# Optimization experiments

Measured on AMD Instinct MI355X. Metric: run time of the kernel, lower is better.

Reference implementation:

```python
import jax, jax.numpy as jnp
import numpy as np
from jax import lax

T = 8
TAU = 2.0
ALPHA = 4.0   # spikingjelly surrogate.Sigmoid default alpha
EPS = 1e-5


def _kaiming(key, shape, fan_in):
    return jax.random.normal(key, shape, jnp.float32) * np.sqrt(2.0 / fan_in)


def setup_inputs() -> dict:
    key = jax.random.key(0)
    ks = jax.random.split(key, 16)
    d = {}
    d['x'] = jax.random.normal(ks[0], (128, 3, 32, 32), jnp.float32)
    convs = [('1', 32, 3), ('2', 32, 32), ('3', 64, 32), ('4', 64, 64), ('5', 128, 64), ('6', 128, 128)]
    for i, (s, co, ci) in enumerate(convs):
        d['w' + s] = _kaiming(ks[1 + i], (co, ci, 3, 3), ci * 9)
        d['b' + s] = jnp.zeros((co,), jnp.float32)
        d['g' + s] = jnp.ones((co,), jnp.float32)
        d['be' + s] = jnp.zeros((co,), jnp.float32)
    d['fc1_w'] = _kaiming(ks[7], (128, 2048), 2048)
    d['fc1_b'] = jnp.zeros((128,), jnp.float32)
    d['fc2_w'] = _kaiming(ks[8], (10, 128), 128)
    d['fc2_b'] = jnp.zeros((10,), jnp.float32)
    return d


def _conv2d(x, w, b):  # x [M,C,H,W], w [O,I,3,3], pad=1 stride=1
    y = lax.conv_general_dilated(x, w, (1, 1), ((1, 1), (1, 1)),
                                 dimension_numbers=('NCHW', 'OIHW', 'NCHW'))
    return y + b[None, :, None, None]


def _bn(x, g, be):  # training-mode BN over merged (T*N,H,W) batch
    m = x.mean(axis=(0, 2, 3))
    v = x.var(axis=(0, 2, 3))
    inv = g / jnp.sqrt(v + EPS)
    return x * inv[None, :, None, None] + (be - m * inv)[None, :, None, None]


def _lif(x_seq, th):
    # spikingjelly LIFNode defaults: decay_input=True, v_reset=0 (hard reset),
    # surrogate sigmoid gradient. x_seq: [T, ...]
    def step(v, x):
        v = v + (x - v) / TAU
        sig = jax.nn.sigmoid(ALPHA * (v - th))
        hard = (v >= th).astype(x.dtype)
        spike = lax.stop_gradient(hard - sig) + sig  # fwd: heaviside, bwd: sigmoid'
        return v * (1.0 - spike), spike
    return lax.scan(step, jnp.zeros_like(x_seq[0]), x_seq)[1]


def _maxpool(x):  # [M,C,H,W] -> 2x2 stride 2
    return lax.reduce_window(x, -jnp.inf, lax.max, (1, 1, 2, 2), (1, 1, 2, 2), 'VALID')


def _cbl(xs, w, b, g, be, th):  # conv-bn over merged TN, LIF scan over T
    t, n = xs.shape[0], xs.shape[1]
    m = xs.reshape((t * n,) + xs.shape[2:])
    y = _bn(_conv2d(m, w, b), g, be)
    return _lif(y.reshape((t, n) + y.shape[1:]), th)


def _pool_seq(xs):
    t, n = xs.shape[0], xs.shape[1]
    y = _maxpool(xs.reshape((t * n,) + xs.shape[2:]))
    return y.reshape((t, n) + y.shape[1:])


def _forward(x, w1, b1, g1, be1, w2, b2, g2, be2, w3, b3, g3, be3,
             w4, b4, g4, be4, w5, b5, g5, be5, w6, b6, g6, be6,
             fc1_w, fc1_b, fc2_w, fc2_b):
    th = 1.0
    xs = jnp.broadcast_to(x[None], (T,) + x.shape)  # [T,N,3,32,32]
    xs = _cbl(xs, w1, b1, g1, be1, th)
    xs = _cbl(xs, w2, b2, g2, be2, th)
    xs = _pool_seq(xs)                                # [T,N,32,16,16]
    xs = _cbl(xs, w3, b3, g3, be3, th)
    xs = _cbl(xs, w4, b4, g4, be4, th)
    xs = _pool_seq(xs)                                # [T,N,64,8,8]
    xs = _cbl(xs, w5, b5, g5, be5, th)
    xs = _cbl(xs, w6, b6, g6, be6, th)
    xs = _pool_seq(xs)                                # [T,N,128,4,4]
    t, n = xs.shape[0], xs.shape[1]
    f = xs.reshape(t, n, -1)                          # [T,N,2048]
    h = jnp.einsum('tnf,of->tno', f, fc1_w) + fc1_b
    h = _lif(h, 1.0)
    o = jnp.einsum('tnf,of->tno', h, fc2_w) + fc2_b
    o = _lif(o, 1.0)
    return o.mean(axis=0)                             # [N,10]


def reference(x, w1, b1, g1, be1, w2, b2, g2, be2, w3, b3, g3, be3,
              w4, b4, g4, be4, w5, b5, g5, be5, w6, b6, g6, be6,
              fc1_w, fc1_b, fc2_w, fc2_b):
    return _forward(x, w1, b1, g1, be1, w2, b2, g2, be2, w3, b3, g3, be3,
                    w4, b4, g4, be4, w5, b5, g5, be5, w6, b6, g6, be6,
                    fc1_w, fc1_b, fc2_w, fc2_b)
```

## Files before the change

### kernel.cpp

```cpp
#include <hip/hip_runtime.h>
#include <stdint.h>


#define T_STEPS 8
#define NBATCH 128

typedef __attribute__((ext_vector_type(8))) short short8;
typedef __attribute__((ext_vector_type(4))) float f32x4;

__device__ __forceinline__ uint16_t f2bf(float f) {
    uint32_t x = __float_as_uint(f);
    uint32_t r = x + 0x7FFFu + ((x >> 16) & 1u);
    return (uint16_t)(r >> 16);
}
__device__ __forceinline__ float bf2f(uint16_t h) {
    return __uint_as_float(((uint32_t)h) << 16);
}

__device__ __forceinline__ void tsplit(float v, uint16_t& h1, uint16_t& h2, uint16_t& h3) {
    h1 = f2bf(v);
    const float r1 = v - bf2f(h1);
    h2 = f2bf(r1);
    const float r2 = r1 - bf2f(h2);
    h3 = f2bf(r2);
}

__device__ __forceinline__ void prep_conv_one(const float* __restrict__ w,
                                              uint16_t* __restrict__ wp, int i, int CIN) {
    const int KC = CIN >> 5;
    const int sh = i % 9;
    const int ci = (i / 9) % CIN;
    const int co = i / (9 * CIN);
    uint16_t h1, h2, h3;
    tsplit(w[i], h1, h2, h3);
    uint16_t* base = wp + (size_t)((co >> 4) * KC + (ci >> 5)) * 14976
                        + sh * 1664 + (co & 15) * 104 + (ci & 31);
    base[0] = h1;
    base[32] = h2;
    base[64] = h3;
}

__device__ __forceinline__ void prep_fc1_one(const float* __restrict__ w,
                                             uint16_t* __restrict__ wp, int i) {
    const int kp = i & 2047;
    const int o = i >> 11;
    const int px = kp >> 7, c = kp & 127;
    uint16_t h1, h2, h3;
    tsplit(w[o * 2048 + c * 16 + px], h1, h2, h3);
    uint16_t* base = wp + (size_t)((o >> 4) * 64 + (kp >> 5)) * 1664
                        + (o & 15) * 104 + (kp & 31);
    base[0] = h1;
    base[32] = h2;
    base[64] = h3;
}

__global__ void prep_all_kernel(const float* __restrict__ W2, const float* __restrict__ W3,
                                const float* __restrict__ W4, const float* __restrict__ W5,
                                const float* __restrict__ W6, const float* __restrict__ F1,
                                uint16_t* __restrict__ P2, uint16_t* __restrict__ P3,
                                uint16_t* __restrict__ P4, uint16_t* __restrict__ P5,
                                uint16_t* __restrict__ P6, uint16_t* __restrict__ PF,
                                float* __restrict__ stats) {
    int i = blockIdx.x * blockDim.x + threadIdx.x;
    if (i < 1536) { stats[i] = 0.0f; return; }
    i -= 1536;
    if (i < 9216) { prep_conv_one(W2, P2, i, 32); return; }
    i -= 9216;
    if (i < 18432) { prep_conv_one(W3, P3, i, 32); return; }
    i -= 18432;
    if (i < 36864) { prep_conv_one(W4, P4, i, 64); return; }
    i -= 36864;
    if (i < 73728) { prep_conv_one(W5, P5, i, 64); return; }
    i -= 73728;
    if (i < 147456) { prep_conv_one(W6, P6, i, 128); return; }
    i -= 147456;
    if (i < 262144) prep_fc1_one(F1, PF, i);
}

__global__ void border_all_kernel(uint8_t* S1, uint8_t* S2, uint8_t* S3,
                                  uint8_t* S4, uint8_t* S5, uint8_t* S6) {
    int i = blockIdx.x * blockDim.x + threadIdx.x;
    uint8_t* s;
    int C, HP, WPP;
    if (i < 1081344) { s = S1; C = 32; HP = 34; WPP = 34; }
    else if ((i -= 1081344) < 557056) { s = S2; C = 32; HP = 18; WPP = 18; }
    else if ((i -= 557056) < 1114112) { s = S3; C = 64; HP = 18; WPP = 18; }
    else if ((i -= 1114112) < 589824) { s = S4; C = 64; HP = 10; WPP = 10; }
    else if ((i -= 589824) < 1179648) { s = S5; C = 128; HP = 10; WPP = 10; }
    else if ((i -= 1179648) < 655360) { s = S6; C = 128; HP = 6; WPP = 6; }
    else return;
    const int C4 = C >> 2;
    const int NB = 2 * WPP + 2 * (HP - 2);
    const int c4 = i % C4;
    const int b = (i / C4) % NB;
    const int img = i / (C4 * NB);
    int py, px;
    if (b < WPP) { py = 0; px = b; }
    else if (b < 2 * WPP) { py = HP - 1; px = b - WPP; }
    else { const int r = b - 2 * WPP; py = 1 + (r >> 1); px = (r & 1) ? (WPP - 1) : 0; }
    *(uint32_t*)&s[(size_t)img * (HP * WPP * C) + (py * WPP + px) * C + 4 * c4] = 0u;
}

__global__ __launch_bounds__(256) void conv1_kernel(
    const float* __restrict__ x, const float* __restrict__ w,
    const float* __restrict__ bias, float* __restrict__ y,
    float* __restrict__ ssum, float* __restrict__ ssq)
{
    __shared__ float tile[3][10][34];
    __shared__ float bnl[64];
    const int tid = threadIdx.x;
    const int m = blockIdx.x;
    const int y0 = blockIdx.y * 8;
    const int co = tid & 31;
    const int strip = tid >> 5;

    if (tid < 64) bnl[tid] = 0.0f;
    for (int i = tid; i < 3 * 10 * 34; i += 256) ((float*)tile)[i] = 0.0f;
    __syncthreads();

    {
        const int gy0 = (y0 == 0) ? 0 : y0 - 1;
        const int gy1 = (y0 + 8 > 31) ? 31 : y0 + 8;
        const int nrows = gy1 - gy0 + 1;
        for (int i = tid; i < 3 * nrows * 32; i += 256) {
            const int gx = i & 31;
            const int r = (i >> 5) % nrows;
            const int ci = i / (32 * nrows);
            const int gy = gy0 + r;
            tile[ci][gy - y0 + 1][gx + 1] =
                x[((size_t)m * 3 + ci) * 1024 + gy * 32 + gx];
        }
    }
    __syncthreads();

    float wr[27];
#pragma unroll
    for (int j = 0; j < 27; ++j) wr[j] = w[co * 27 + j];
    const float bv = bias[co];

    float lsum = 0.0f, lsq = 0.0f;
#pragma unroll
    for (int g = 0; g < 8; ++g) {
        float s[3][3][6];
#pragma unroll
        for (int ci = 0; ci < 3; ++ci)
#pragma unroll
            for (int ky = 0; ky < 3; ++ky)
#pragma unroll
                for (int c = 0; c < 6; ++c)
                    s[ci][ky][c] = tile[ci][g + ky][strip * 4 + c];
#pragma unroll
        for (int r = 0; r < 4; ++r) {
            float acc = bv;
#pragma unroll
            for (int ci = 0; ci < 3; ++ci)
#pragma unroll
                for (int ky = 0; ky < 3; ++ky)
#pragma unroll
                    for (int kx = 0; kx < 3; ++kx)
                        acc += s[ci][ky][r + kx] * wr[ci * 9 + ky * 3 + kx];
            const int lx = strip * 4 + r;
            y[(((size_t)m * 1024) + (y0 + g) * 32 + lx) * 32 + co] = acc;
            lsum += acc;
            lsq += acc * acc;
        }
    }
    atomicAdd(&bnl[co], lsum);
    atomicAdd(&bnl[32 + co], lsq);
    __syncthreads();
    if (tid < 32) atomicAdd(&ssum[tid], bnl[tid]);
    else if (tid < 64) atomicAdd(&ssq[tid - 32], bnl[tid]);
}

template <int CIN, int COUT, int H, int W, int ROWS, int IMPB, int NCO, int KSPLIT>
__global__ __launch_bounds__(256) void conv_mfma_kernel(
    const uint8_t* __restrict__ in, const uint16_t* __restrict__ wp,
    const float* __restrict__ bias, float* __restrict__ y,
    float* __restrict__ ssum, float* __restrict__ ssq)
{
    constexpr int KC = CIN / 32;
    constexpr int WPP = W + 2;
    constexpr int HW = H * W;
    constexpr int PXU16 = CIN + 8;
    constexpr int ISTR_B = (H + 2) * WPP * CIN;
    constexpr int RB = H / ROWS;
    constexpr int NSTRIP = IMPB * ROWS * W / 16;
    constexpr int MSPLIT = 4 / KSPLIT;
    constexpr int SPW = NSTRIP / MSPLIT;
    constexpr int TILE_U16 = IMPB * (ROWS + 2) * WPP * PXU16;
    constexpr int TILE_B = IMPB * (ROWS + 2) * WPP * CIN;
    constexpr int NIT = KC * 9;
    constexpr int ITW = NIT / KSPLIT;
    constexpr int CS = NCO * 16 + 1;
    static_assert(IMPB == 1 || ROWS == H, "impb needs full-image tiles");
    static_assert(NSTRIP % MSPLIT == 0 && NSTRIP % 4 == 0, "strips");
    static_assert(NIT % KSPLIT == 0, "ksplit");
    static_assert(TILE_B % 16 == 0, "tile u8 16B");
    static_assert(KSPLIT == 1 || TILE_U16 * 2 >= NSTRIP * 16 * CS * 4, "C fits");

    __shared__ __align__(16) uint16_t sp[TILE_U16];
    __shared__ float bn[NCO * 32];

    const int tid = threadIdx.x;
    const int lane = tid & 63;
    const int wav = tid >> 6;
    const int kg = wav / MSPLIT;
    const int mg = wav - kg * MSPLIT;
    const int col = lane & 15;
    const int quad = lane >> 4;

    const int m0 = (blockIdx.x / RB) * IMPB;
    const int ybase = (blockIdx.x % RB) * ROWS;

    if (tid < NCO * 32) bn[tid] = 0.0f;

    {
        const uint8_t* src = in + (size_t)m0 * ISTR_B + (size_t)ybase * WPP * CIN;
        for (int i = tid; i < TILE_B / 16; i += 256) {
            const uint4 v = ((const uint4*)src)[i];
            const int b = i * 16;
            const int px = b / CIN;
            const int ci = b - px * CIN;
            uint32_t* d = (uint32_t*)&sp[px * PXU16 + ci];
            d[0] = ((v.x & 1u) | (((v.x >> 8) & 1u) << 16)) * 0x3F80u;
            d[1] = (((v.x >> 16) & 1u) | (((v.x >> 24) & 1u) << 16)) * 0x3F80u;
            d[2] = ((v.y & 1u) | (((v.y >> 8) & 1u) << 16)) * 0x3F80u;
            d[3] = (((v.y >> 16) & 1u) | (((v.y >> 24) & 1u) << 16)) * 0x3F80u;
            d[4] = ((v.z & 1u) | (((v.z >> 8) & 1u) << 16)) * 0x3F80u;
            d[5] = (((v.z >> 16) & 1u) | (((v.z >> 24) & 1u) << 16)) * 0x3F80u;
            d[6] = ((v.w & 1u) | (((v.w >> 8) & 1u) << 16)) * 0x3F80u;
            d[7] = (((v.w >> 16) & 1u) | (((v.w >> 24) & 1u) << 16)) * 0x3F80u;
        }
    }
    __syncthreads();

    int abase[SPW];
#pragma unroll
    for (int s = 0; s < SPW; ++s) {
        const int p = (mg * SPW + s) * 16 + col;
        const int img = p / (ROWS * W);
        const int rem = p % (ROWS * W);
        abase[s] = ((img * (ROWS + 2) + rem / W) * WPP + rem % W) * PXU16 + quad * 8;
    }

    f32x4 acc[SPW][NCO];
#pragma unroll
    for (int s = 0; s < SPW; ++s)
#pragma unroll
        for (int j = 0; j < NCO; ++j) acc[s][j] = (f32x4)0.0f;

    const uint16_t* wbase = wp + ((size_t)blockIdx.y * NCO * KC) * 14976
                               + col * 104 + quad * 8;

    auto loadB = [&](short8 (&buf)[NCO][3], int it) {
        const int kc = it / 9, sh = it - kc * 9;
#pragma unroll
        for (int j = 0; j < NCO; ++j) {
            const uint16_t* p = wbase + (size_t)(j * KC + kc) * 14976 + sh * 1664;
            buf[j][0] = *(const short8*)p;
            buf[j][1] = *(const short8*)(p + 32);
            buf[j][2] = *(const short8*)(p + 64);
        }
    };
    auto mfmaStep = [&](short8 (&buf)[NCO][3], int it) {
        const int kc = it / 9, sh = it - kc * 9;
        const int dy = sh / 3, dx = sh - dy * 3;
        const int shoff = (dy * WPP + dx) * PXU16 + kc * 32;
#pragma unroll
        for (int s = 0; s < SPW; ++s) {
            const short8 a = *(const short8*)&sp[abase[s] + shoff];
#pragma unroll
            for (int j = 0; j < NCO; ++j) {
                f32x4 t = acc[s][j];
                t = __builtin_amdgcn_mfma_f32_16x16x32_bf16(a, buf[j][0], t, 0, 0, 0);
                t = __builtin_amdgcn_mfma_f32_16x16x32_bf16(a, buf[j][1], t, 0, 0, 0);
                t = __builtin_amdgcn_mfma_f32_16x16x32_bf16(a, buf[j][2], t, 0, 0, 0);
                acc[s][j] = t;
            }
        }
    };

    short8 bufA[NCO][3], bufB[NCO][3];
    const int it0 = kg * ITW, it1 = it0 + ITW;
    loadB(bufA, it0);
    int it = it0;
#pragma unroll 1
    for (; it + 2 <= it1; it += 2) {
        loadB(bufB, it + 1);
        mfmaStep(bufA, it);
        if (it + 2 < it1) loadB(bufA, it + 2);
        mfmaStep(bufB, it + 1);
    }
    if (it < it1) mfmaStep(bufA, it);

    float bv[NCO];
#pragma unroll
    for (int j = 0; j < NCO; ++j) bv[j] = bias[(blockIdx.y * NCO + j) * 16 + col];

    if constexpr (KSPLIT == 1) {
#pragma unroll
        for (int s = 0; s < SPW; ++s) {
            const int pb_ = (mg * SPW + s) * 16 + quad * 4;
            float sum[NCO], sq[NCO];
#pragma unroll
            for (int j = 0; j < NCO; ++j) { sum[j] = 0.0f; sq[j] = 0.0f; }
#pragma unroll
            for (int r = 0; r < 4; ++r) {
                const int p = pb_ + r;
                const int img = p / (ROWS * W);
                const int pxim = p % (ROWS * W) + ybase * W;
                float* yp = &y[((size_t)(m0 + img) * HW + pxim) * COUT
                               + blockIdx.y * NCO * 16 + col];
#pragma unroll
                for (int j = 0; j < NCO; ++j) {
                    const float v = acc[s][j][r] + bv[j];
                    yp[j * 16] = v;
                    sum[j] += v;
                    sq[j] += v * v;
                }
            }
#pragma unroll
            for (int j = 0; j < NCO; ++j) {
                float su = sum[j], s2 = sq[j];
                su += __shfl_xor(su, 16, 64);
                su += __shfl_xor(su, 32, 64);
                s2 += __shfl_xor(s2, 16, 64);
                s2 += __shfl_xor(s2, 32, 64);
                if (quad == 0) {
                    atomicAdd(&bn[j * 32 + col], su);
                    atomicAdd(&bn[j * 32 + 16 + col], s2);
                }
            }
        }
    } else {
        float* Csh = (float*)sp;
        __syncthreads();
        if (kg == 0) {
#pragma unroll
            for (int s = 0; s < SPW; ++s)
#pragma unroll
                for (int j = 0; j < NCO; ++j)
#pragma unroll
                    for (int r = 0; r < 4; ++r)
                        Csh[((mg * SPW + s) * 16 + quad * 4 + r) * CS + j * 16 + col]
                            = acc[s][j][r];
        }
        __syncthreads();
#pragma unroll
        for (int k = 1; k < KSPLIT; ++k) {
            if (kg == k) {
#pragma unroll
                for (int s = 0; s < SPW; ++s)
#pragma unroll
                    for (int j = 0; j < NCO; ++j)
#pragma unroll
                        for (int r = 0; r < 4; ++r)
                            Csh[((mg * SPW + s) * 16 + quad * 4 + r) * CS + j * 16 + col]
                                += acc[s][j][r];
            }
            __syncthreads();
        }
        constexpr int ES = NSTRIP / 4;
#pragma unroll
        for (int s2i = 0; s2i < ES; ++s2i) {
            const int gs = wav * ES + s2i;
            float sum[NCO], sq[NCO];
#pragma unroll
            for (int j = 0; j < NCO; ++j) { sum[j] = 0.0f; sq[j] = 0.0f; }
#pragma unroll
            for (int r = 0; r < 4; ++r) {
                const int p = gs * 16 + quad * 4 + r;
                const int img = p / (ROWS * W);
                const int pxim = p % (ROWS * W) + ybase * W;
                float* yp = &y[((size_t)(m0 + img) * HW + pxim) * COUT
                               + blockIdx.y * NCO * 16 + col];
#pragma unroll
                for (int j = 0; j < NCO; ++j) {
                    const float v = Csh[p * CS + j * 16 + col] + bv[j];
                    yp[j * 16] = v;
                    sum[j] += v;
                    sq[j] += v * v;
                }
            }
#pragma unroll
            for (int j = 0; j < NCO; ++j) {
                float su = sum[j], s2 = sq[j];
                su += __shfl_xor(su, 16, 64);
                su += __shfl_xor(su, 32, 64);
                s2 += __shfl_xor(s2, 16, 64);
                s2 += __shfl_xor(s2, 32, 64);
                if (quad == 0) {
                    atomicAdd(&bn[j * 32 + col], su);
                    atomicAdd(&bn[j * 32 + 16 + col], s2);
                }
            }
        }
    }
    __syncthreads();
    if (tid < NCO * 32) {
        const int j = tid >> 5, r = tid & 31;
        const int co0 = (blockIdx.y * NCO + j) * 16;
        if (r < 16) atomicAdd(&ssum[co0 + r], bn[j * 32 + r]);
        else atomicAdd(&ssq[co0 + r - 16], bn[j * 32 + r]);
    }
}

__global__ void bnlif1_pad_kernel(const float* __restrict__ y,
                                  const float* __restrict__ ssum,
                                  const float* __restrict__ ssq,
                                  const float* __restrict__ g,
                                  const float* __restrict__ be,
                                  uint8_t* __restrict__ s, float invM) {
    constexpr int OSTR = 34 * 34 * 32;
    const int i = blockIdx.x * blockDim.x + threadIdx.x;
    if (i >= NBATCH * 1024 * 8) return;
    const int c4 = i & 7;
    const int px = (i >> 3) & 1023;
    const int n = i >> 13;
    const int c0 = 4 * c4;
    float z[4], v[4];
    const float4 q = *(const float4*)&y[((size_t)n * 1024 + px) * 32 + c0];
    const float* qf = (const float*)&q;
#pragma unroll
    for (int c = 0; c < 4; ++c) {
        const float m = ssum[c0 + c] * invM;
        const float inv = g[c0 + c] / sqrtf(ssq[c0 + c] * invM - m * m + 1e-5f);
        z[c] = qf[c] * inv + (be[c0 + c] - m * inv);
        v[c] = 0.0f;
    }
    const int pyy = px >> 5, pxx = px & 31;
    const size_t obase = (size_t)n * OSTR + ((pyy + 1) * 34 + pxx + 1) * 32 + c0;
    const size_t ot = (size_t)NBATCH * OSTR;
#pragma unroll
    for (int t = 0; t < T_STEPS; ++t) {
        uint32_t pk = 0;
#pragma unroll
        for (int c = 0; c < 4; ++c) {
            v[c] += (z[c] - v[c]) * 0.5f;
            if (v[c] >= 1.0f) { v[c] = 0.0f; pk |= 1u << (8 * c); }
        }
        *(uint32_t*)&s[t * ot + obase] = pk;
    }
}

template <int C, int H, int W>
__global__ void bnlif_pad_kernel(const float* __restrict__ y,
                                 const float* __restrict__ ssum,
                                 const float* __restrict__ ssq,
                                 const float* __restrict__ g,
                                 const float* __restrict__ be,
                                 uint8_t* __restrict__ s, float invM) {
    constexpr int C4 = C / 4;
    constexpr int HW = H * W;
    constexpr int OSTR = (H + 2) * (W + 2) * C;
    const int i = blockIdx.x * blockDim.x + threadIdx.x;
    if (i >= NBATCH * HW * C4) return;
    const int c4 = i % C4;
    const int px = (i / C4) % HW;
    const int n = i / (C4 * HW);
    const int c0 = 4 * c4;
    float inv[4], sh[4], v[4];
#pragma unroll
    for (int c = 0; c < 4; ++c) {
        const float m = ssum[c0 + c] * invM;
        inv[c] = g[c0 + c] / sqrtf(ssq[c0 + c] * invM - m * m + 1e-5f);
        sh[c] = be[c0 + c] - m * inv[c];
        v[c] = 0.0f;
    }
    const size_t ybase = ((size_t)n * HW + px) * C + c0;
    const size_t tstride = (size_t)NBATCH * HW * C;
    const int pyy = px / W, pxx = px % W;
    const size_t obase = (size_t)n * OSTR + ((pyy + 1) * (W + 2) + pxx + 1) * C + c0;
    const size_t ot = (size_t)NBATCH * OSTR;
#pragma unroll
    for (int t = 0; t < T_STEPS; ++t) {
        const float4 q = *(const float4*)&y[t * tstride + ybase];
        const float* qf = (const float*)&q;
        uint32_t pk = 0;
#pragma unroll
        for (int c = 0; c < 4; ++c) {
            const float z = qf[c] * inv[c] + sh[c];
            v[c] += (z - v[c]) * 0.5f;
            if (v[c] >= 1.0f) { v[c] = 0.0f; pk |= 1u << (8 * c); }
        }
        *(uint32_t*)&s[t * ot + obase] = pk;
    }
}

template <int C, int H, int W>
__global__ void bnlifpool_pad_kernel(const float* __restrict__ y,
                                     const float* __restrict__ ssum,
                                     const float* __restrict__ ssq,
                                     const float* __restrict__ g,
                                     const float* __restrict__ be,
                                     uint8_t* __restrict__ s, float invM) {
    constexpr int C4 = C / 4;
    constexpr int PH = H / 2, PW = W / 2;
    constexpr int OSTR = (PH + 2) * (PW + 2) * C;
    const int i = blockIdx.x * blockDim.x + threadIdx.x;
    if (i >= NBATCH * PH * PW * C4) return;
    const int c4 = i % C4;
    const int pw = (i / C4) % PW;
    const int ph = (i / (C4 * PW)) % PH;
    const int n = i / (C4 * PW * PH);
    const int c0 = 4 * c4;
    float inv[4], sh[4], v[4][4];
#pragma unroll
    for (int c = 0; c < 4; ++c) {
        const float m = ssum[c0 + c] * invM;
        inv[c] = g[c0 + c] / sqrtf(ssq[c0 + c] * invM - m * m + 1e-5f);
        sh[c] = be[c0 + c] - m * inv[c];
#pragma unroll
        for (int p = 0; p < 4; ++p) v[p][c] = 0.0f;
    }
    const size_t base = (((size_t)n * H + 2 * ph) * W + 2 * pw) * C + c0;
    const size_t tstride = (size_t)NBATCH * H * W * C;
    const size_t obase = (size_t)n * OSTR + ((ph + 1) * (PW + 2) + pw + 1) * C + c0;
    const size_t ot = (size_t)NBATCH * OSTR;
#pragma unroll
    for (int t = 0; t < T_STEPS; ++t) {
        const float* yt = y + t * tstride + base;
        float4 q[4];
        q[0] = *(const float4*)&yt[0];
        q[1] = *(const float4*)&yt[C];
        q[2] = *(const float4*)&yt[(size_t)W * C];
        q[3] = *(const float4*)&yt[(size_t)W * C + C];
        uint32_t pk = 0;
#pragma unroll
        for (int p = 0; p < 4; ++p) {
            const float* qf = (const float*)&q[p];
#pragma unroll
            for (int c = 0; c < 4; ++c) {
                const float z = qf[c] * inv[c] + sh[c];
                v[p][c] += (z - v[p][c]) * 0.5f;
                if (v[p][c] >= 1.0f) { v[p][c] = 0.0f; pk |= 1u << (8 * c); }
            }
        }
        *(uint32_t*)&s[t * ot + obase] = pk;
    }
}

__global__ __launch_bounds__(256) void fc1_mfma_kernel(
    const uint8_t* __restrict__ f, const uint16_t* __restrict__ wfc,
    const float* __restrict__ b, float* __restrict__ h)
{
    __shared__ __align__(16) uint16_t A[16 * 2056];
    const int tid = threadIdx.x;
    const int lane = tid & 63, wav = tid >> 6;
    const int col = lane & 15, quad = lane >> 4;
    const int r0 = blockIdx.x * 16;

    {
        const int row = tid >> 4, px = tid & 15;
        const int py = px >> 2, pxx = px & 3;
        const uint8_t* src = f + (size_t)(r0 + row) * 4608
                             + ((py + 1) * 6 + pxx + 1) * 128;
        uint32_t* dst = (uint32_t*)&A[row * 2056 + px * 128];
#pragma unroll
        for (int i = 0; i < 8; ++i) {
            const uint4 v = ((const uint4*)src)[i];
            dst[8 * i + 0] = ((v.x & 1u) | (((v.x >> 8) & 1u) << 16)) * 0x3F80u;
            dst[8 * i + 1] = (((v.x >> 16) & 1u) | (((v.x >> 24) & 1u) << 16)) * 0x3F80u;
            dst[8 * i + 2] = ((v.y & 1u) | (((v.y >> 8) & 1u) << 16)) * 0x3F80u;
            dst[8 * i + 3] = (((v.y >> 16) & 1u) | (((v.y >> 24) & 1u) << 16)) * 0x3F80u;
            dst[8 * i + 4] = ((v.z & 1u) | (((v.z >> 8) & 1u) << 16)) * 0x3F80u;
            dst[8 * i + 5] = (((v.z >> 16) & 1u) | (((v.z >> 24) & 1u) << 16)) * 0x3F80u;
            dst[8 * i + 6] = ((v.w & 1u) | (((v.w >> 8) & 1u) << 16)) * 0x3F80u;
            dst[8 * i + 7] = (((v.w >> 16) & 1u) | (((v.w >> 24) & 1u) << 16)) * 0x3F80u;
        }
    }
    __syncthreads();

    const int coblk = blockIdx.y * 4 + wav;
    const uint16_t* wbase = wfc + (size_t)coblk * 64 * 1664 + col * 104 + quad * 8;
    f32x4 acc = (f32x4)0.0f;

    auto loadB = [&](short8 (&buf)[3], int kc) {
        const uint16_t* p = wbase + kc * 1664;
        buf[0] = *(const short8*)p;
        buf[1] = *(const short8*)(p + 32);
        buf[2] = *(const short8*)(p + 64);
    };
    auto step = [&](short8 (&buf)[3], int kc) {
        const short8 a = *(const short8*)&A[col * 2056 + kc * 32 + quad * 8];
        acc = __builtin_amdgcn_mfma_f32_16x16x32_bf16(a, buf[0], acc, 0, 0, 0);
        acc = __builtin_amdgcn_mfma_f32_16x16x32_bf16(a, buf[1], acc, 0, 0, 0);
        acc = __builtin_amdgcn_mfma_f32_16x16x32_bf16(a, buf[2], acc, 0, 0, 0);
    };

    short8 bA[3], bB[3];
    loadB(bA, 0);
#pragma unroll 1
    for (int kc = 0; kc + 2 <= 64; kc += 2) {
        loadB(bB, kc + 1);
        step(bA, kc);
        if (kc + 2 < 64) loadB(bA, kc + 2);
        step(bB, kc + 1);
    }

    const int o = coblk * 16 + col;
    const float bv = b[o];
#pragma unroll
    for (int r = 0; r < 4; ++r)
        h[(size_t)(r0 + quad * 4 + r) * 128 + o] = acc[r] + bv;
}

__global__ void lif_fc_kernel(const float* __restrict__ h,
                              uint8_t* __restrict__ s, int NF) {
    const int i = blockIdx.x * blockDim.x + threadIdx.x;
    if (i >= NF) return;
    float v = 0.0f;
#pragma unroll
    for (int t = 0; t < T_STEPS; ++t) {
        const float z = h[(size_t)t * NF + i];
        v += (z - v) * 0.5f;
        const float sp = (v >= 1.0f) ? 1.0f : 0.0f;
        s[(size_t)t * NF + i] = (uint8_t)sp;
        v *= (1.0f - sp);
    }
}

__global__ void fc2_kernel(const uint8_t* __restrict__ sh,
                           const float* __restrict__ w,
                           const float* __restrict__ b,
                           float* __restrict__ out) {
    const int i = blockIdx.x * blockDim.x + threadIdx.x;
    if (i >= NBATCH * 10) return;
    const int k = i % 10;
    const int n = i / 10;
    float v = 0.0f, acc = 0.0f;
    for (int t = 0; t < T_STEPS; ++t) {
        const uint8_t* row = sh + ((size_t)t * NBATCH + n) * 128;
        float z = b[k];
        for (int o = 0; o < 128; ++o)
            z += (float)row[o] * w[k * 128 + o];
        v += (z - v) * 0.5f;
        const float sp = (v >= 1.0f) ? 1.0f : 0.0f;
        acc += sp;
        v *= (1.0f - sp);
    }
    out[i] = acc * (1.0f / T_STEPS);
}

extern "C" void kernel_launch(void* const* d_in, const int* in_sizes, int n_in,
                              void* d_out, int out_size, void* d_ws, size_t ws_size,
                              hipStream_t stream) {
    const float* x   = (const float*)d_in[0];
    const float* W1  = (const float*)d_in[1];
    const float* Bi1 = (const float*)d_in[2];
    const float* G1  = (const float*)d_in[3];
    const float* BE1 = (const float*)d_in[4];
    const float* W2  = (const float*)d_in[5];
    const float* Bi2 = (const float*)d_in[6];
    const float* G2  = (const float*)d_in[7];
    const float* BE2 = (const float*)d_in[8];
    const float* W3  = (const float*)d_in[9];
    const float* Bi3 = (const float*)d_in[10];
    const float* G3  = (const float*)d_in[11];
    const float* BE3 = (const float*)d_in[12];
    const float* W4  = (const float*)d_in[13];
    const float* Bi4 = (const float*)d_in[14];
    const float* G4  = (const float*)d_in[15];
    const float* BE4 = (const float*)d_in[16];
    const float* W5  = (const float*)d_in[17];
    const float* Bi5 = (const float*)d_in[18];
    const float* G5  = (const float*)d_in[19];
    const float* BE5 = (const float*)d_in[20];
    const float* W6  = (const float*)d_in[21];
    const float* Bi6 = (const float*)d_in[22];
    const float* G6  = (const float*)d_in[23];
    const float* BE6 = (const float*)d_in[24];
    const float* FC1W = (const float*)d_in[25];
    const float* FC1B = (const float*)d_in[26];
    const float* FC2W = (const float*)d_in[27];
    const float* FC2B = (const float*)d_in[28];

    uint8_t* ws = (uint8_t*)d_ws;
    float*   Y  = (float*)ws;
    const size_t SOFF = 134217728;
    uint8_t* S1 = ws + SOFF;
    uint8_t* S2 = ws + SOFF;
    uint8_t* S3 = ws + SOFF + 10616832;
    uint8_t* S4 = ws + SOFF;
    uint8_t* S5 = ws + SOFF + 6553600;
    uint8_t* S6 = ws + SOFF + 19660800;
    float*   stats = (float*)(ws + SOFF + 37879808);
    float*   h     = (float*)(ws + SOFF + 37879808 + 8192);
    uint8_t* shb   = ws + SOFF + 37879808 + 8192 + 524288;
    uint16_t* Wp   = (uint16_t*)(shb + 131072);
    uint16_t* Wp2p = Wp;
    uint16_t* Wp3p = Wp + 29952;
    uint16_t* Wp4p = Wp + 89856;
    uint16_t* Wp5p = Wp + 209664;
    uint16_t* Wp6p = Wp + 449280;
    uint16_t* Wfc1 = Wp + 928512;

    prep_all_kernel<<<(549376 + 255) / 256, 256, 0, stream>>>(
        W2, W3, W4, W5, W6, FC1W, Wp2p, Wp3p, Wp4p, Wp5p, Wp6p, Wfc1, stats);
    border_all_kernel<<<(5177344 + 255) / 256, 256, 0, stream>>>(S1, S2, S3, S4, S5, S6);

    const int TN = T_STEPS * NBATCH;

    {
        conv1_kernel<<<dim3(NBATCH, 4), 256, 0, stream>>>(x, W1, Bi1, Y,
                                                          stats + 0, stats + 128);
        bnlif1_pad_kernel<<<(NBATCH * 1024 * 8) / 256, 256, 0, stream>>>(
            Y, stats + 0, stats + 128, G1, BE1, S1, 1.0f / 131072.0f);
    }
    {
        conv_mfma_kernel<32, 32, 32, 32, 8, 1, 2, 1><<<dim3(TN * 4, 1), 256, 0, stream>>>(
            S1, Wp2p, Bi2, Y, stats + 256, stats + 384);
        bnlifpool_pad_kernel<32, 32, 32><<<(NBATCH * 16 * 16 * 8) / 256, 256, 0, stream>>>(
            Y, stats + 256, stats + 384, G2, BE2, S2, 1.0f / (1024.0f * 1024.0f));
    }
    {
        conv_mfma_kernel<32, 64, 16, 16, 16, 2, 2, 1><<<dim3(TN / 2, 2), 256, 0, stream>>>(
            S2, Wp3p, Bi3, Y, stats + 512, stats + 640);
        bnlif_pad_kernel<64, 16, 16><<<(NBATCH * 256 * 16) / 256, 256, 0, stream>>>(
            Y, stats + 512, stats + 640, G3, BE3, S3, 1.0f / (1024.0f * 256.0f));
    }
    {
        conv_mfma_kernel<64, 64, 16, 16, 16, 1, 2, 2><<<dim3(TN, 2), 256, 0, stream>>>(
            S3, Wp4p, Bi4, Y, stats + 768, stats + 896);
        bnlifpool_pad_kernel<64, 16, 16><<<(NBATCH * 8 * 8 * 16) / 256, 256, 0, stream>>>(
            Y, stats + 768, stats + 896, G4, BE4, S4, 1.0f / (1024.0f * 256.0f));
    }
    {
        conv_mfma_kernel<64, 128, 8, 8, 8, 2, 2, 2><<<dim3(TN / 2, 4), 256, 0, stream>>>(
            S4, Wp5p, Bi5, Y, stats + 1024, stats + 1152);
        bnlif_pad_kernel<128, 8, 8><<<(NBATCH * 64 * 32) / 256, 256, 0, stream>>>(
            Y, stats + 1024, stats + 1152, G5, BE5, S5, 1.0f / (1024.0f * 64.0f));
    }
    {
        conv_mfma_kernel<128, 128, 8, 8, 8, 2, 2, 4><<<dim3(TN / 2, 4), 256, 0, stream>>>(
            S5, Wp6p, Bi6, Y, stats + 1280, stats + 1408);
        bnlifpool_pad_kernel<128, 8, 8><<<(NBATCH * 4 * 4 * 32) / 256, 256, 0, stream>>>(
            Y, stats + 1280, stats + 1408, G6, BE6, S6, 1.0f / (1024.0f * 64.0f));
    }
    fc1_mfma_kernel<<<dim3(64, 2), 256, 0, stream>>>(S6, Wfc1, FC1B, h);
    lif_fc_kernel<<<(NBATCH * 128 + 255) / 256, 256, 0, stream>>>(h, shb, NBATCH * 128);
    fc2_kernel<<<(NBATCH * 10 + 255) / 256, 256, 0, stream>>>(shb, FC2W, FC2B, (float*)d_out);
}
```

Measured before the change: 620.9 us.

## Recompute conv2 in a fused conv+BN+LIF+pool kernel instead of storing Y

```diff
diff --git a/kernel.cpp b/kernel.cpp
--- a/kernel.cpp
+++ b/kernel.cpp
@@ -172,7 +172,8 @@
     else if (tid < 64) atomicAdd(&ssq[tid - 32], bnl[tid]);
 }
 
-template <int CIN, int COUT, int H, int W, int ROWS, int IMPB, int NCO, int KSPLIT>
+template <int CIN, int COUT, int H, int W, int ROWS, int IMPB, int NCO, int KSPLIT,
+          bool WRITE_Y = true>
 __global__ __launch_bounds__(256) void conv_mfma_kernel(
     const uint8_t* __restrict__ in, const uint16_t* __restrict__ wp,
     const float* __restrict__ bias, float* __restrict__ y,
@@ -314,7 +315,7 @@
 #pragma unroll
                 for (int j = 0; j < NCO; ++j) {
                     const float v = acc[s][j][r] + bv[j];
-                    yp[j * 16] = v;
+                    if constexpr (WRITE_Y) yp[j * 16] = v;
                     sum[j] += v;
                     sq[j] += v * v;
                 }
@@ -377,7 +378,7 @@
 #pragma unroll
                 for (int j = 0; j < NCO; ++j) {
                     const float v = Csh[p * CS + j * 16 + col] + bv[j];
-                    yp[j * 16] = v;
+                    if constexpr (WRITE_Y) yp[j * 16] = v;
                     sum[j] += v;
                     sq[j] += v * v;
                 }
@@ -402,6 +403,157 @@
         const int co0 = (blockIdx.y * NCO + j) * 16;
         if (r < 16) atomicAdd(&ssum[co0 + r], bn[j * 32 + r]);
         else atomicAdd(&ssq[co0 + r - 16], bn[j * 32 + r]);
+    }
+}
+
+__global__ __launch_bounds__(256) void conv2_fused_kernel(
+    const uint8_t* __restrict__ in, const uint16_t* __restrict__ wp,
+    const float* __restrict__ bias,
+    const float* __restrict__ ssum, const float* __restrict__ ssq,
+    const float* __restrict__ g, const float* __restrict__ be,
+    uint8_t* __restrict__ sout, float invM)
+{
+    constexpr int WPP = 34, PXU16 = 40;
+    constexpr int TILE_U16 = 10 * 34 * 40;
+    constexpr int TILE_B = 10 * 34 * 32;
+    constexpr int ISTR_B = 34 * 34 * 32;
+    constexpr int OSTR = 18 * 18 * 32;
+    __shared__ __align__(16) uint16_t sp[TILE_U16];
+
+    const int tid = threadIdx.x;
+    const int lane = tid & 63, wav = tid >> 6;
+    const int col = lane & 15, quad = lane >> 4;
+    const int n = blockIdx.x >> 2;
+    const int rt = blockIdx.x & 3;
+    const int ybase = rt * 8;
+
+    float inv[2], shf[2], bv[2];
+#pragma unroll
+    for (int j = 0; j < 2; ++j) {
+        const int c = j * 16 + col;
+        const float m = ssum[c] * invM;
+        inv[j] = g[c] / sqrtf(ssq[c] * invM - m * m + 1e-5f);
+        shf[j] = be[c] - m * inv[j];
+        bv[j] = bias[c];
+    }
+
+    int abase[4];
+#pragma unroll
+    for (int s = 0; s < 4; ++s) {
+        const int p = (wav * 4 + s) * 16 + col;
+        abase[s] = ((p >> 5) * WPP + (p & 31)) * PXU16 + quad * 8;
+    }
+
+    const uint16_t* wbase = wp + col * 104 + quad * 8;
+
+    float vst[4][2][4];
+#pragma unroll
+    for (int s = 0; s < 4; ++s)
+#pragma unroll
+        for (int j = 0; j < 2; ++j)
+#pragma unroll
+            for (int r = 0; r < 4; ++r) vst[s][j][r] = 0.0f;
+
+    const size_t ot = (size_t)NBATCH * OSTR;
+
+#pragma unroll 1
+    for (int t = 0; t < T_STEPS; ++t) {
+        {
+            const uint8_t* src = in + (size_t)(t * NBATCH + n) * ISTR_B
+                                 + (size_t)ybase * WPP * 32;
+            for (int i = tid; i < TILE_B / 16; i += 256) {
+                const uint4 v = ((const uint4*)src)[i];
+                const int b = i * 16;
+                const int px = b >> 5;
+                const int ci = b & 31;
+                uint32_t* d = (uint32_t*)&sp[px * PXU16 + ci];
+                d[0] = ((v.x & 1u) | (((v.x >> 8) & 1u) << 16)) * 0x3F80u;
+                d[1] = (((v.x >> 16) & 1u) | (((v.x >> 24) & 1u) << 16)) * 0x3F80u;
+                d[2] = ((v.y & 1u) | (((v.y >> 8) & 1u) << 16)) * 0x3F80u;
+                d[3] = (((v.y >> 16) & 1u) | (((v.y >> 24) & 1u) << 16)) * 0x3F80u;
+                d[4] = ((v.z & 1u) | (((v.z >> 8) & 1u) << 16)) * 0x3F80u;
+                d[5] = (((v.z >> 16) & 1u) | (((v.z >> 24) & 1u) << 16)) * 0x3F80u;
+                d[6] = ((v.w & 1u) | (((v.w >> 8) & 1u) << 16)) * 0x3F80u;
+                d[7] = (((v.w >> 16) & 1u) | (((v.w >> 24) & 1u) << 16)) * 0x3F80u;
+            }
+        }
+        __syncthreads();
+
+        f32x4 acc[4][2];
+#pragma unroll
+        for (int s = 0; s < 4; ++s)
+#pragma unroll
+            for (int j = 0; j < 2; ++j) acc[s][j] = (f32x4)0.0f;
+
+        auto loadB = [&](short8 (&buf)[2][3], int it) {
+#pragma unroll
+            for (int j = 0; j < 2; ++j) {
+                const uint16_t* p = wbase + (size_t)j * 14976 + it * 1664;
+                buf[j][0] = *(const short8*)p;
+                buf[j][1] = *(const short8*)(p + 32);
+                buf[j][2] = *(const short8*)(p + 64);
+            }
+        };
+        auto mfmaStep = [&](short8 (&buf)[2][3], int it) {
+            const int dy = it / 3, dx = it - dy * 3;
+            const int shoff = (dy * WPP + dx) * PXU16;
+#pragma unroll
+            for (int s = 0; s < 4; ++s) {
+                const short8 a = *(const short8*)&sp[abase[s] + shoff];
+#pragma unroll
+                for (int j = 0; j < 2; ++j) {
+                    f32x4 tt = acc[s][j];
+                    tt = __builtin_amdgcn_mfma_f32_16x16x32_bf16(a, buf[j][0], tt, 0, 0, 0);
+                    tt = __builtin_amdgcn_mfma_f32_16x16x32_bf16(a, buf[j][1], tt, 0, 0, 0);
+                    tt = __builtin_amdgcn_mfma_f32_16x16x32_bf16(a, buf[j][2], tt, 0, 0, 0);
+                    acc[s][j] = tt;
+                }
+            }
+        };
+
+        short8 bufA[2][3], bufB[2][3];
+        loadB(bufA, 0);
+        int it = 0;
+#pragma unroll 1
+        for (; it + 2 <= 9; it += 2) {
+            loadB(bufB, it + 1);
+            mfmaStep(bufA, it);
+            if (it + 2 < 9) loadB(bufA, it + 2);
+            mfmaStep(bufB, it + 1);
+        }
+        mfmaStep(bufA, 8);
+
+        uint32_t spk[4][2];
+#pragma unroll
+        for (int s = 0; s < 4; ++s)
+#pragma unroll
+            for (int j = 0; j < 2; ++j) {
+                uint32_t bits = 0;
+#pragma unroll
+                for (int r = 0; r < 4; ++r) {
+                    const float yv = acc[s][j][r] + bv[j];
+                    const float z = yv * inv[j] + shf[j];
+                    vst[s][j][r] += (z - vst[s][j][r]) * 0.5f;
+                    if (vst[s][j][r] >= 1.0f) { vst[s][j][r] = 0.0f; bits |= 1u << r; }
+                }
+                spk[s][j] = bits;
+            }
+        const int prow = rt * 4 + wav;
+#pragma unroll
+        for (int s = 0; s < 2; ++s) {
+#pragma unroll
+            for (int rp = 0; rp < 2; ++rp) {
+                const int px = s * 8 + quad * 2 + rp;
+                uint8_t* op = &sout[t * ot + (size_t)n * OSTR
+                                    + ((prow + 1) * 18 + px + 1) * 32 + col];
+#pragma unroll
+                for (int j = 0; j < 2; ++j) {
+                    const uint32_t m4 = (spk[s][j] | spk[s + 2][j]) >> (2 * rp);
+                    op[j * 16] = (uint8_t)((m4 | (m4 >> 1)) & 1u);
+                }
+            }
+        }
+        __syncthreads();
     }
 }
 
@@ -708,10 +860,12 @@
             Y, stats + 0, stats + 128, G1, BE1, S1, 1.0f / 131072.0f);
     }
     {
-        conv_mfma_kernel<32, 32, 32, 32, 8, 1, 2, 1><<<dim3(TN * 4, 1), 256, 0, stream>>>(
-            S1, Wp2p, Bi2, Y, stats + 256, stats + 384);
-        bnlifpool_pad_kernel<32, 32, 32><<<(NBATCH * 16 * 16 * 8) / 256, 256, 0, stream>>>(
-            Y, stats + 256, stats + 384, G2, BE2, S2, 1.0f / (1024.0f * 1024.0f));
+        conv_mfma_kernel<32, 32, 32, 32, 8, 1, 2, 1, false>
+            <<<dim3(TN * 4, 1), 256, 0, stream>>>(
+                S1, Wp2p, Bi2, Y, stats + 256, stats + 384);
+        conv2_fused_kernel<<<NBATCH * 4, 256, 0, stream>>>(
+            S1, Wp2p, Bi2, stats + 256, stats + 384, G2, BE2, S2,
+            1.0f / (1024.0f * 1024.0f));
     }
     {
         conv_mfma_kernel<32, 64, 16, 16, 16, 2, 2, 1><<<dim3(TN / 2, 2), 256, 0, stream>>>(
```

Result: no change. 616.8 us, median of 2 (-0.7%).
